# Kernel tuning notes

Hardware: AMD Instinct MI355X
Metric: run time of the kernel (lower is better)

The kernel has to match this reference:

```python
import jax, jax.numpy as jnp
import numpy as np
import math

D_MODEL = 1024
NUM_HEADS = 16
MAX_LEN = 2048
D_HEAD = D_MODEL // NUM_HEADS
BATCH = 2
SEQ = 2048


def setup_inputs() -> dict:
    root = jax.random.key(0)
    ks = jax.random.split(root, 10)
    s = 1.0 / math.sqrt(D_MODEL)
    return {
        "query": jax.random.normal(ks[0], (BATCH, SEQ, D_MODEL), jnp.float32),
        "key": jax.random.normal(ks[1], (BATCH, SEQ, D_MODEL), jnp.float32),
        "value": jax.random.normal(ks[2], (BATCH, SEQ, D_MODEL), jnp.float32),
        "Wq": jax.random.normal(ks[3], (D_MODEL, D_MODEL), jnp.float32) * s,
        "bq": jax.random.normal(ks[4], (D_MODEL,), jnp.float32) * s,
        "Wk": jax.random.normal(ks[5], (D_MODEL, D_MODEL), jnp.float32) * s,
        "bk": jax.random.normal(ks[6], (D_MODEL,), jnp.float32) * s,
        "Wv": jax.random.normal(ks[7], (D_MODEL, D_MODEL), jnp.float32) * s,
        "bv": jax.random.normal(ks[8], (D_MODEL,), jnp.float32) * s,
        "Er": jax.random.normal(ks[9], (MAX_LEN, D_HEAD), jnp.float32),
    }


def _skew(QEr):
    # QEr: [B, H, S, S] -> pad one zero column on the left, reshape, drop first row
    B, H, R, C = QEr.shape
    padded = jnp.pad(QEr, ((0, 0), (0, 0), (0, 0), (1, 0)))  # [B,H,R,C+1]
    reshaped = padded.reshape(B, H, C + 1, R)
    return reshaped[:, :, 1:, :]  # [B,H,R,C] == Srel


def reference(query, key, value, Wq, bq, Wk, bk, Wv, bv, Er):
    B, S, D = query.shape
    H, dh = NUM_HEADS, D_HEAD
    # nn.Linear: x @ W.T + b
    q = (jnp.einsum("bsd,ed->bse", query, Wq) + bq).reshape(B, S, H, dh).transpose(0, 2, 1, 3)  # [B,H,S,dh]
    k = (jnp.einsum("bsd,ed->bse", key, Wk) + bk).reshape(B, S, H, dh).transpose(0, 2, 1, 3)
    v = (jnp.einsum("bsd,ed->bse", value, Wv) + bv).reshape(B, S, H, dh).transpose(0, 2, 1, 3)
    start = MAX_LEN - S
    Er_s = Er[start:, :]  # [S, dh]
    QEr = jnp.einsum("bhsd,ld->bhsl", q, Er_s)  # [B,H,S,S]
    Srel = _skew(QEr)
    QK = jnp.einsum("bhsd,bhtd->bhst", q, k)
    attn = (QK + Srel) / math.sqrt(dh)
    causal = jnp.tril(jnp.ones((S, S), dtype=bool))
    attn = jnp.where(causal[None, None], attn, -jnp.inf)
    attn = jax.nn.softmax(attn, axis=-1)
    out = jnp.einsum("bhst,bhtd->bhsd", attn, v)  # [B,H,S,dh]
    out = out.transpose(0, 2, 1, 3).reshape(B, S, D)
    return out  # dropout is identity in eval mode
```

## Files before the change

kernel.cpp:

```cpp
#include <hip/hip_runtime.h>
#include <hip/hip_bf16.h>

typedef __attribute__((ext_vector_type(8))) short bf16x8;
typedef __attribute__((ext_vector_type(4))) float f32x4;

#define DEVI __device__ __forceinline__

constexpr int SEQ_   = 2048;
constexpr int HEADS  = 16;
constexpr int DHEAD  = 64;
constexpr int DMODEL = 1024;

DEVI unsigned short f2bf(float x) {
  __hip_bfloat16 h = __float2bfloat16(x);
  return __builtin_bit_cast(unsigned short, h);
}

DEVI f32x4 MFMA(bf16x8 a, bf16x8 b, f32x4 c) {
  return __builtin_amdgcn_mfma_f32_16x16x32_bf16(a, b, c, 0, 0, 0);
}

__global__ void conv3_kernel(const float* s0, const float* s1, const float* s2,
                             unsigned short* d0, unsigned short* d1, unsigned short* d2,
                             int n) {
  const float* s = (blockIdx.y == 0) ? s0 : (blockIdx.y == 1) ? s1 : s2;
  unsigned short* d = (blockIdx.y == 0) ? d0 : (blockIdx.y == 1) ? d1 : d2;
  int i = (blockIdx.x * 256 + threadIdx.x) * 8;
  if (i >= n) return;
  const float4* p = (const float4*)(s + i);
  float4 v0 = p[0], v1 = p[1];
  union { unsigned short u[8]; bf16x8 v; } t;
  t.u[0] = f2bf(v0.x); t.u[1] = f2bf(v0.y); t.u[2] = f2bf(v0.z); t.u[3] = f2bf(v0.w);
  t.u[4] = f2bf(v1.x); t.u[5] = f2bf(v1.y); t.u[6] = f2bf(v1.z); t.u[7] = f2bf(v1.w);
  *(bf16x8*)(d + i) = t.v;
}

__global__ void conv4_kernel(const float* s0, const float* s1, const float* s2,
                             const float* s3,
                             unsigned short* d0, unsigned short* d1,
                             unsigned short* d2, unsigned short* d3,
                             int n_w, int n_e) {
  const int y = blockIdx.y;
  const float* s = (y == 0) ? s0 : (y == 1) ? s1 : (y == 2) ? s2 : s3;
  unsigned short* d = (y == 0) ? d0 : (y == 1) ? d1 : (y == 2) ? d2 : d3;
  const int n = (y == 3) ? n_e : n_w;
  int i = (blockIdx.x * 256 + threadIdx.x) * 8;
  if (i >= n) return;
  const float4* p = (const float4*)(s + i);
  float4 v0 = p[0], v1 = p[1];
  union { unsigned short u[8]; bf16x8 v; } t;
  t.u[0] = f2bf(v0.x); t.u[1] = f2bf(v0.y); t.u[2] = f2bf(v0.z); t.u[3] = f2bf(v0.w);
  t.u[4] = f2bf(v1.x); t.u[5] = f2bf(v1.y); t.u[6] = f2bf(v1.z); t.u[7] = f2bf(v1.w);
  *(bf16x8*)(d + i) = t.v;
}

__global__ __launch_bounds__(256) void proj3_kernel(
    const unsigned short* __restrict__ X0, const unsigned short* __restrict__ X1,
    const unsigned short* __restrict__ X2,
    const unsigned short* __restrict__ W0, const unsigned short* __restrict__ W1,
    const unsigned short* __restrict__ W2,
    const float* __restrict__ bi0, const float* __restrict__ bi1,
    const float* __restrict__ bi2,
    unsigned short* __restrict__ o0, unsigned short* __restrict__ o1,
    unsigned short* __restrict__ o2) {
  const int z = blockIdx.z;
  const unsigned short* X = (z == 0) ? X0 : (z == 1) ? X1 : X2;
  const unsigned short* W = (z == 0) ? W0 : (z == 1) ? W1 : W2;
  const float* bias        = (z == 0) ? bi0 : (z == 1) ? bi1 : bi2;
  unsigned short* out      = (z == 0) ? o0 : (z == 1) ? o1 : o2;

  __shared__ unsigned short Abuf[2][128 * 32];
  __shared__ unsigned short Bbuf[2][128 * 32];
  const int tid  = threadIdx.x;
  const int lane = tid & 63, wv = tid >> 6;
  const int q = lane >> 4, r = lane & 15;
  const int wrow = wv >> 1, wcol = wv & 1;
  const int rowA0 = blockIdx.x * 128, colB0 = blockIdx.y * 128;

  const char* Ag = (const char*)(X + (size_t)rowA0 * DMODEL);
  const char* Bg = (const char*)(W + (size_t)colB0 * DMODEL);

  f32x4 acc[4][4] = {};

  auto stage = [&](int ks, int buf) {
    const int koff = ks * 64;
#pragma unroll
    for (int i = 0; i < 2; ++i) {
      const int b   = (i * 256 + tid) * 16;
      const int row = b >> 6, col = b & 63;
      __builtin_amdgcn_global_load_lds(
          (const __attribute__((address_space(1))) void*)(Ag + (size_t)row * (DMODEL * 2) + koff + col),
          (__attribute__((address_space(3))) void*)((char*)&Abuf[buf][0] + i * 4096 + wv * 1024),
          16, 0, 0);
      __builtin_amdgcn_global_load_lds(
          (const __attribute__((address_space(1))) void*)(Bg + (size_t)row * (DMODEL * 2) + koff + col),
          (__attribute__((address_space(3))) void*)((char*)&Bbuf[buf][0] + i * 4096 + wv * 1024),
          16, 0, 0);
    }
  };

  stage(0, 0);
  for (int ks = 0; ks < 32; ++ks) {
    __syncthreads();
    if (ks + 1 < 32) stage(ks + 1, (ks + 1) & 1);
    const unsigned short* A  = &Abuf[ks & 1][0];
    const unsigned short* Bt = &Bbuf[ks & 1][0];
    bf16x8 af[4], bfr[4];
#pragma unroll
    for (int t = 0; t < 4; ++t) {
      af[t]  = *(const bf16x8*)(A  + (wrow * 64 + t * 16 + r) * 32 + q * 8);
      bfr[t] = *(const bf16x8*)(Bt + (wcol * 64 + t * 16 + r) * 32 + q * 8);
    }
#pragma unroll
    for (int m = 0; m < 4; ++m)
#pragma unroll
      for (int n = 0; n < 4; ++n)
        acc[m][n] = MFMA(af[m], bfr[n], acc[m][n]);
  }

#pragma unroll
  for (int m = 0; m < 4; ++m) {
#pragma unroll
    for (int n = 0; n < 4; ++n) {
      const int e  = colB0 + wcol * 64 + n * 16 + r;
      const float bv = bias[e];
      const int h = e >> 6, dd = e & 63;
      const int nrow0 = rowA0 + wrow * 64 + m * 16 + q * 4;
      const int bb = nrow0 >> 11, ss0 = nrow0 & 2047;
      const size_t bh = (size_t)(bb * HEADS + h);
      if (z == 0) {
#pragma unroll
        for (int j = 0; j < 4; ++j)
          out[(bh * SEQ_ + (ss0 + j)) * DHEAD + dd] = f2bf((acc[m][n][j] + bv) * 0.125f);
      } else if (z == 1) {
#pragma unroll
        for (int j = 0; j < 4; ++j) {
          const int s = ss0 + j;
          const size_t off = (bh * 64 + (size_t)(s >> 5)) * 2048
                           + (size_t)(((dd >> 5) * 2 + ((s >> 4) & 1)) * 512)
                           + (size_t)(((((dd & 31) >> 3) << 4) + (s & 15)) * 8)
                           + (dd & 7);
          out[off] = f2bf(acc[m][n][j] + bv);
        }
      } else {
        union { unsigned short u[4]; uint2 v; } pk;
#pragma unroll
        for (int j = 0; j < 4; ++j) pk.u[j] = f2bf(acc[m][n][j] + bv);
        const size_t off = (bh * 64 + (size_t)(ss0 >> 5)) * 2048
                         + (size_t)((dd >> 4) * 512)
                         + (size_t)(((((ss0 & 31) >> 3) << 4) + (dd & 15)) * 8)
                         + (ss0 & 7);
        *(uint2*)&out[off] = pk.v;
      }
    }
  }
}

struct ErF { bf16x8 e10, e11, e20, e21; };

__global__ __launch_bounds__(512, 4) void attn_kernel(
    const unsigned short* __restrict__ qb, const unsigned short* __restrict__ kt,
    const unsigned short* __restrict__ vt, const unsigned short* __restrict__ Er,
    float* __restrict__ out) {
  __shared__ unsigned short k_lds[2][2048];
  __shared__ unsigned short v_lds[2][2048];
  __shared__ unsigned short p_lds[8][16][40];

  const int tid  = threadIdx.x;
  const int lane = tid & 63, wv = tid >> 6;
  const int q = lane >> 4, r = lane & 15;

  const int lid = blockIdx.x;
  const int xcd = lid & 7, idx = lid >> 3;
  const int bh  = (xcd << 2) | (idx & 3);
  const int T   = 15 - (idx >> 2);
  const int s0  = T * 128 + wv * 16;
  const int nIter = 4 * T + 4;
  const int bb = bh >> 4, hh = bh & 15;

  const unsigned short* qbh = qb + (size_t)bh * SEQ_ * DHEAD;
  const char* ktb = (const char*)(kt + (size_t)bh * 64 * 2048);
  const char* vtb = (const char*)(vt + (size_t)bh * 64 * 2048);
  const f32x4 zero4 = {0.f, 0.f, 0.f, 0.f};

  const bool isK = (tid < 256);
  const char* sbase = isK ? ktb : vtb;
  const int subt = tid & 255;

  auto stage = [&](int tile, int buf) {
    char* dst = (char*)(isK ? &k_lds[buf][0] : &v_lds[buf][0]) + (wv & 3) * 1024;
    __builtin_amdgcn_global_load_lds(
        (const __attribute__((address_space(1))) void*)(sbase + (size_t)tile * 4096 + subt * 16),
        (__attribute__((address_space(3))) void*)dst, 16, 0, 0);
  };

  auto loadE = [&](ErF& e, int it2) {
    const int lb = 2032 + it2 * 32 - s0;
    int l1 = lb + 16 + r; l1 = l1 < 2047 ? l1 : 2047;
    int l2 = lb + 32 + r; l2 = l2 < 2047 ? l2 : 2047;
    e.e10 = *(const bf16x8*)(Er + (size_t)l1 * DHEAD + q * 8);
    e.e11 = *(const bf16x8*)(Er + (size_t)l1 * DHEAD + 32 + q * 8);
    e.e20 = *(const bf16x8*)(Er + (size_t)l2 * DHEAD + q * 8);
    e.e21 = *(const bf16x8*)(Er + (size_t)l2 * DHEAD + 32 + q * 8);
  };

  stage(0, 0);
  bf16x8 qf0 = *(const bf16x8*)(qbh + (size_t)(s0 + r) * DHEAD + q * 8);
  bf16x8 qf1 = *(const bf16x8*)(qbh + (size_t)(s0 + r) * DHEAD + 32 + q * 8);

  f32x4 oacc[4] = {};
  float lpart[4] = {0.f, 0.f, 0.f, 0.f};
  f32x4 qer0;
  {
    const int l0 = 2032 - s0 + r;
    bf16x8 e00 = *(const bf16x8*)(Er + (size_t)l0 * DHEAD + q * 8);
    bf16x8 e01 = *(const bf16x8*)(Er + (size_t)l0 * DHEAD + 32 + q * 8);
    qer0 = MFMA(qf1, e01, MFMA(qf0, e00, zero4));
  }

  auto body = [&](int it, int cur, const ErF& e) {
    const int t0 = it * 32;
    if (t0 > s0 + 15) return;
    const unsigned short* KL = &k_lds[cur][0];
    const unsigned short* VL = &v_lds[cur][0];
    bf16x8 kf00 = *(const bf16x8*)(KL + lane * 8);
    bf16x8 kf10 = *(const bf16x8*)(KL + 512 + lane * 8);
    bf16x8 kf01 = *(const bf16x8*)(KL + 1024 + lane * 8);
    bf16x8 kf11 = *(const bf16x8*)(KL + 1536 + lane * 8);

    __builtin_amdgcn_s_setprio(1);
    f32x4 s40  = MFMA(qf1, kf01, MFMA(qf0, kf00, zero4));
    f32x4 s41  = MFMA(qf1, kf11, MFMA(qf0, kf10, zero4));
    f32x4 qer1 = MFMA(qf1, e.e11, MFMA(qf0, e.e10, zero4));
    f32x4 qer2 = MFMA(qf1, e.e21, MFMA(qf0, e.e20, zero4));
    __builtin_amdgcn_s_setprio(0);

    const int d0 = t0 - s0;
#pragma unroll
    for (int j = 0; j < 4; ++j) {
      const int sl = q * 4 + j;
      const int idxw = r + 15 - sl;
      const int srcl = (q << 4) | (idxw & 15);
      const float g0s = __shfl(qer0[j], srcl);
      const float g1s = __shfl(qer1[j], srcl);
      const float g2s = __shfl(qer2[j], srcl);
      const bool lo = (idxw < 16);
      const float sv0 = s40[j] + (lo ? g0s : g1s);
      const float sv1 = s41[j] + (lo ? g1s : g2s);
      const int a = sl - r;
      const float p0 = (a >= d0)      ? __expf(sv0) : 0.f;
      const float p1 = (a >= d0 + 16) ? __expf(sv1) : 0.f;
      lpart[j] += p0 + p1;
      p_lds[wv][sl][r]      = f2bf(p0);
      p_lds[wv][sl][16 + r] = f2bf(p1);
    }

    bf16x8 pf  = *(const bf16x8*)(&p_lds[wv][r][0] + q * 8);
    bf16x8 vf0 = *(const bf16x8*)(VL + lane * 8);
    bf16x8 vf1 = *(const bf16x8*)(VL + 512 + lane * 8);
    bf16x8 vf2 = *(const bf16x8*)(VL + 1024 + lane * 8);
    bf16x8 vf3 = *(const bf16x8*)(VL + 1536 + lane * 8);
    __builtin_amdgcn_s_setprio(1);
    oacc[0] = MFMA(pf, vf0, oacc[0]);
    oacc[1] = MFMA(pf, vf1, oacc[1]);
    oacc[2] = MFMA(pf, vf2, oacc[2]);
    oacc[3] = MFMA(pf, vf3, oacc[3]);
    __builtin_amdgcn_s_setprio(0);
    qer0 = qer2;
  };

  ErF eA, eB;
  loadE(eA, 0);
  int it = 0;
  while (true) {
    __syncthreads();
    if (it + 1 < nIter) { stage(it + 1, 1); loadE(eB, it + 1); }
    body(it, 0, eA);
    if (++it >= nIter) break;
    __syncthreads();
    if (it + 1 < nIter) { stage(it + 1, 0); loadE(eA, it + 1); }
    body(it, 1, eB);
    if (++it >= nIter) break;
  }

#pragma unroll
  for (int j = 0; j < 4; ++j) {
    float ls = lpart[j];
#pragma unroll
    for (int d = 1; d < 16; d <<= 1) ls += __shfl_xor(ls, d);
    const float inv = 1.0f / ls;
    const int ss = s0 + q * 4 + j;
#pragma unroll
    for (int dc = 0; dc < 4; ++dc) {
      const int dd = dc * 16 + r;
      out[((size_t)(bb * SEQ_ + ss)) * DMODEL + hh * DHEAD + dd] = oacc[dc][j] * inv;
    }
  }
}

extern "C" void kernel_launch(void* const* d_in, const int* in_sizes, int n_in,
                              void* d_out, int out_size, void* d_ws, size_t ws_size,
                              hipStream_t stream) {
  const float* query = (const float*)d_in[0];
  const float* key   = (const float*)d_in[1];
  const float* value = (const float*)d_in[2];
  const float* Wq    = (const float*)d_in[3];
  const float* bq    = (const float*)d_in[4];
  const float* Wk    = (const float*)d_in[5];
  const float* bk    = (const float*)d_in[6];
  const float* Wv    = (const float*)d_in[7];
  const float* bv    = (const float*)d_in[8];
  const float* Er    = (const float*)d_in[9];

  char* ws = (char*)d_ws;
  unsigned short* qb   = (unsigned short*)(ws + (0u  << 20));
  unsigned short* ktil = (unsigned short*)(ws + (8u  << 20));
  unsigned short* vtil = (unsigned short*)(ws + (16u << 20));
  unsigned short* Xq   = (unsigned short*)(ws + (32u << 20));
  unsigned short* Xk   = (unsigned short*)(ws + (40u << 20));
  unsigned short* Xv   = (unsigned short*)(ws + (48u << 20));
  unsigned short* Wqb  = (unsigned short*)(ws + (56u << 20));
  unsigned short* Wkb  = (unsigned short*)(ws + (58u << 20));
  unsigned short* Wvb  = (unsigned short*)(ws + (60u << 20));
  unsigned short* Erb  = (unsigned short*)(ws + (62u << 20));

  conv3_kernel<<<dim3(2048, 3), 256, 0, stream>>>(query, key, value, Xq, Xk, Xv,
                                                  2 * SEQ_ * DMODEL);
  conv4_kernel<<<dim3(512, 4), 256, 0, stream>>>(Wq, Wk, Wv, Er,
                                                 Wqb, Wkb, Wvb, Erb,
                                                 DMODEL * DMODEL, SEQ_ * DHEAD);

  proj3_kernel<<<dim3(32, 8, 3), 256, 0, stream>>>(Xq, Xk, Xv, Wqb, Wkb, Wvb,
                                                   bq, bk, bv, qb, ktil, vtil);

  attn_kernel<<<dim3(512), 512, 0, stream>>>(qb, ktil, vtil, Erb, (float*)d_out);
}
```

Before: 163.8 us.

## Retile attention to 32-row waves, 64-key tiles, and triple-buffered KV loads

The attention kernel now uses 4 waves of 32 query rows each, in place of 8 waves of 16 rows, and processes 64 keys per iteration instead of 32. Each K/V fragment loaded from LDS is therefore reused across two row tiles, and there are half as many iterations and barriers. KV staging moves to a 3-deep LDS ring, with a manual vmcnt wait plus s_barrier replacing __syncthreads so prefetches can stay in flight. In exchange it uses more registers and LDS, and has fewer waves per block and per CU, which may hurt latency hiding.

Result: faster. 144.5 us (-11.8%).

```diff
diff --git a/kernel.cpp b/kernel.cpp
--- a/kernel.cpp
+++ b/kernel.cpp
@@ -5,6 +5,8 @@
 typedef __attribute__((ext_vector_type(4))) float f32x4;
 
 #define DEVI __device__ __forceinline__
+#define AS1 __attribute__((address_space(1)))
+#define AS3 __attribute__((address_space(3)))
 
 constexpr int SEQ_   = 2048;
 constexpr int HEADS  = 16;
@@ -89,12 +91,12 @@
       const int b   = (i * 256 + tid) * 16;
       const int row = b >> 6, col = b & 63;
       __builtin_amdgcn_global_load_lds(
-          (const __attribute__((address_space(1))) void*)(Ag + (size_t)row * (DMODEL * 2) + koff + col),
-          (__attribute__((address_space(3))) void*)((char*)&Abuf[buf][0] + i * 4096 + wv * 1024),
+          (const AS1 void*)(Ag + (size_t)row * (DMODEL * 2) + koff + col),
+          (AS3 void*)((char*)&Abuf[buf][0] + i * 4096 + wv * 1024),
           16, 0, 0);
       __builtin_amdgcn_global_load_lds(
-          (const __attribute__((address_space(1))) void*)(Bg + (size_t)row * (DMODEL * 2) + koff + col),
-          (__attribute__((address_space(3))) void*)((char*)&Bbuf[buf][0] + i * 4096 + wv * 1024),
+          (const AS1 void*)(Bg + (size_t)row * (DMODEL * 2) + koff + col),
+          (AS3 void*)((char*)&Bbuf[buf][0] + i * 4096 + wv * 1024),
           16, 0, 0);
     }
   };
@@ -156,15 +158,13 @@
   }
 }
 
-struct ErF { bf16x8 e10, e11, e20, e21; };
-
-__global__ __launch_bounds__(512, 4) void attn_kernel(
+__global__ __launch_bounds__(256, 2) void attn_kernel(
     const unsigned short* __restrict__ qb, const unsigned short* __restrict__ kt,
     const unsigned short* __restrict__ vt, const unsigned short* __restrict__ Er,
     float* __restrict__ out) {
-  __shared__ unsigned short k_lds[2][2048];
-  __shared__ unsigned short v_lds[2][2048];
-  __shared__ unsigned short p_lds[8][16][40];
+  __shared__ unsigned short k_lds[3][4096];
+  __shared__ unsigned short v_lds[3][4096];
+  __shared__ unsigned short p_lds[4][32][72];
 
   const int tid  = threadIdx.x;
   const int lane = tid & 63, wv = tid >> 6;
@@ -174,8 +174,8 @@
   const int xcd = lid & 7, idx = lid >> 3;
   const int bh  = (xcd << 2) | (idx & 3);
   const int T   = 15 - (idx >> 2);
-  const int s0  = T * 128 + wv * 16;
-  const int nIter = 4 * T + 4;
+  const int s0  = T * 128 + wv * 32;
+  const int nIter = 2 * T + 2;
   const int bb = bh >> 4, hh = bh & 15;
 
   const unsigned short* qbh = qb + (size_t)bh * SEQ_ * DHEAD;
@@ -183,119 +183,173 @@
   const char* vtb = (const char*)(vt + (size_t)bh * 64 * 2048);
   const f32x4 zero4 = {0.f, 0.f, 0.f, 0.f};
 
-  const bool isK = (tid < 256);
-  const char* sbase = isK ? ktb : vtb;
-  const int subt = tid & 255;
-
-  auto stage = [&](int tile, int buf) {
-    char* dst = (char*)(isK ? &k_lds[buf][0] : &v_lds[buf][0]) + (wv & 3) * 1024;
-    __builtin_amdgcn_global_load_lds(
-        (const __attribute__((address_space(1))) void*)(sbase + (size_t)tile * 4096 + subt * 16),
-        (__attribute__((address_space(3))) void*)dst, 16, 0, 0);
+  const char* sgbase = (wv < 2) ? ktb : vtb;
+  char* sdst0 = (char*)((wv < 2) ? &k_lds[0][0] : &v_lds[0][0]);
+  const int shalf = (wv & 1) * 4096;
+  const int soff  = lane * 16;
+
+  auto stageKV = [&](int it, int buf) {
+    const int g = (it < nIter) ? it : nIter - 1;
+    const char* src = sgbase + (size_t)g * 8192 + shalf + soff;
+    char* dst = sdst0 + buf * 8192 + shalf;
+#pragma unroll
+    for (int c = 0; c < 4; ++c)
+      __builtin_amdgcn_global_load_lds((const AS1 void*)(src + c * 1024),
+                                       (AS3 void*)(dst + c * 1024), 16, 0, 0);
   };
 
-  auto loadE = [&](ErF& e, int it2) {
-    const int lb = 2032 + it2 * 32 - s0;
-    int l1 = lb + 16 + r; l1 = l1 < 2047 ? l1 : 2047;
-    int l2 = lb + 32 + r; l2 = l2 < 2047 ? l2 : 2047;
-    e.e10 = *(const bf16x8*)(Er + (size_t)l1 * DHEAD + q * 8);
-    e.e11 = *(const bf16x8*)(Er + (size_t)l1 * DHEAD + 32 + q * 8);
-    e.e20 = *(const bf16x8*)(Er + (size_t)l2 * DHEAD + q * 8);
-    e.e21 = *(const bf16x8*)(Er + (size_t)l2 * DHEAD + 32 + q * 8);
+  struct ErSet { bf16x8 e[8]; };
+  auto loadE = [&](ErSet& es, int it) {
+    const int lb = 2016 + it * 64 - s0;
+#pragma unroll
+    for (int mi = 0; mi < 4; ++mi) {
+      int l = lb + 32 + mi * 16 + r;
+      l = l < 2047 ? l : 2047;
+      es.e[mi * 2 + 0] = *(const bf16x8*)(Er + (size_t)l * DHEAD + q * 8);
+      es.e[mi * 2 + 1] = *(const bf16x8*)(Er + (size_t)l * DHEAD + 32 + q * 8);
+    }
   };
 
-  stage(0, 0);
-  bf16x8 qf0 = *(const bf16x8*)(qbh + (size_t)(s0 + r) * DHEAD + q * 8);
-  bf16x8 qf1 = *(const bf16x8*)(qbh + (size_t)(s0 + r) * DHEAD + 32 + q * 8);
-
-  f32x4 oacc[4] = {};
-  float lpart[4] = {0.f, 0.f, 0.f, 0.f};
-  f32x4 qer0;
+  bf16x8 qf[2][2];
+#pragma unroll
+  for (int rt = 0; rt < 2; ++rt) {
+    qf[rt][0] = *(const bf16x8*)(qbh + (size_t)(s0 + rt * 16 + r) * DHEAD + q * 8);
+    qf[rt][1] = *(const bf16x8*)(qbh + (size_t)(s0 + rt * 16 + r) * DHEAD + 32 + q * 8);
+  }
+  stageKV(0, 0);
+
+  f32x4 qer[2][6];
   {
-    const int l0 = 2032 - s0 + r;
-    bf16x8 e00 = *(const bf16x8*)(Er + (size_t)l0 * DHEAD + q * 8);
-    bf16x8 e01 = *(const bf16x8*)(Er + (size_t)l0 * DHEAD + 32 + q * 8);
-    qer0 = MFMA(qf1, e01, MFMA(qf0, e00, zero4));
-  }
-
-  auto body = [&](int it, int cur, const ErF& e) {
-    const int t0 = it * 32;
-    if (t0 > s0 + 15) return;
+    const int lb = 2016 - s0;
+#pragma unroll
+    for (int m = 0; m < 2; ++m) {
+      const int l = lb + m * 16 + r;
+      bf16x8 e0 = *(const bf16x8*)(Er + (size_t)l * DHEAD + q * 8);
+      bf16x8 e1 = *(const bf16x8*)(Er + (size_t)l * DHEAD + 32 + q * 8);
+#pragma unroll
+      for (int rt = 0; rt < 2; ++rt)
+        qer[rt][m] = MFMA(qf[rt][1], e1, MFMA(qf[rt][0], e0, zero4));
+    }
+  }
+
+  f32x4 oacc[2][4] = {};
+  float lpart[2][4] = {};
+
+  ErSet eA, eB;
+  loadE(eA, 0);
+
+  auto body = [&](int it, int cur, const ErSet& es) {
+    const int t0 = it * 64;
+    if (t0 > s0 + 31) return;
     const unsigned short* KL = &k_lds[cur][0];
     const unsigned short* VL = &v_lds[cur][0];
-    bf16x8 kf00 = *(const bf16x8*)(KL + lane * 8);
-    bf16x8 kf10 = *(const bf16x8*)(KL + 512 + lane * 8);
-    bf16x8 kf01 = *(const bf16x8*)(KL + 1024 + lane * 8);
-    bf16x8 kf11 = *(const bf16x8*)(KL + 1536 + lane * 8);
-
+
+    bf16x8 kf[4][2];
+#pragma unroll
+    for (int ct = 0; ct < 4; ++ct)
+#pragma unroll
+      for (int kc = 0; kc < 2; ++kc)
+        kf[ct][kc] = *(const bf16x8*)(KL + (ct >> 1) * 2048 + (kc * 2 + (ct & 1)) * 512 + lane * 8);
+
+    f32x4 s4[2][4];
     __builtin_amdgcn_s_setprio(1);
-    f32x4 s40  = MFMA(qf1, kf01, MFMA(qf0, kf00, zero4));
-    f32x4 s41  = MFMA(qf1, kf11, MFMA(qf0, kf10, zero4));
-    f32x4 qer1 = MFMA(qf1, e.e11, MFMA(qf0, e.e10, zero4));
-    f32x4 qer2 = MFMA(qf1, e.e21, MFMA(qf0, e.e20, zero4));
+#pragma unroll
+    for (int rt = 0; rt < 2; ++rt)
+#pragma unroll
+      for (int ct = 0; ct < 4; ++ct)
+        s4[rt][ct] = MFMA(qf[rt][1], kf[ct][1], MFMA(qf[rt][0], kf[ct][0], zero4));
+#pragma unroll
+    for (int rt = 0; rt < 2; ++rt)
+#pragma unroll
+      for (int mi = 0; mi < 4; ++mi)
+        qer[rt][2 + mi] = MFMA(qf[rt][1], es.e[mi * 2 + 1],
+                               MFMA(qf[rt][0], es.e[mi * 2 + 0], zero4));
     __builtin_amdgcn_s_setprio(0);
 
     const int d0 = t0 - s0;
 #pragma unroll
+    for (int rt = 0; rt < 2; ++rt) {
+#pragma unroll
+      for (int j = 0; j < 4; ++j) {
+        const int srcl = (q << 4) | ((15 + r - q * 4 - j) & 15);
+        float g0 = __shfl(qer[rt][1 - rt][j], srcl);
+        float g1 = __shfl(qer[rt][2 - rt][j], srcl);
+        float g2 = __shfl(qer[rt][3 - rt][j], srcl);
+        float g3 = __shfl(qer[rt][4 - rt][j], srcl);
+        float g4 = __shfl(qer[rt][5 - rt][j], srcl);
+        const bool hi = (r > q * 4 + j);
+        const float b0 = hi ? g1 : g0;
+        const float b1 = hi ? g2 : g1;
+        const float b2 = hi ? g3 : g2;
+        const float b3 = hi ? g4 : g3;
+        const int A_ = rt * 16 + q * 4 + j - r - d0;
+        const float p0 = (A_ >= 0)  ? __expf(s4[rt][0][j] + b0) : 0.f;
+        const float p1 = (A_ >= 16) ? __expf(s4[rt][1][j] + b1) : 0.f;
+        const float p2 = (A_ >= 32) ? __expf(s4[rt][2][j] + b2) : 0.f;
+        const float p3 = (A_ >= 48) ? __expf(s4[rt][3][j] + b3) : 0.f;
+        lpart[rt][j] += (p0 + p1) + (p2 + p3);
+        const int sl = rt * 16 + q * 4 + j;
+        p_lds[wv][sl][r]      = f2bf(p0);
+        p_lds[wv][sl][16 + r] = f2bf(p1);
+        p_lds[wv][sl][32 + r] = f2bf(p2);
+        p_lds[wv][sl][48 + r] = f2bf(p3);
+      }
+    }
+
+    bf16x8 vf[4][2];
+#pragma unroll
+    for (int dc = 0; dc < 4; ++dc)
+#pragma unroll
+      for (int tc = 0; tc < 2; ++tc)
+        vf[dc][tc] = *(const bf16x8*)(VL + tc * 2048 + dc * 512 + lane * 8);
+    __builtin_amdgcn_s_setprio(1);
+#pragma unroll
+    for (int rt = 0; rt < 2; ++rt) {
+      bf16x8 pf0 = *(const bf16x8*)(&p_lds[wv][rt * 16 + r][0] + q * 8);
+      bf16x8 pf1 = *(const bf16x8*)(&p_lds[wv][rt * 16 + r][0] + 32 + q * 8);
+#pragma unroll
+      for (int dc = 0; dc < 4; ++dc)
+        oacc[rt][dc] = MFMA(pf1, vf[dc][1], MFMA(pf0, vf[dc][0], oacc[rt][dc]));
+    }
+    __builtin_amdgcn_s_setprio(0);
+
+#pragma unroll
+    for (int rt = 0; rt < 2; ++rt) { qer[rt][0] = qer[rt][4]; qer[rt][1] = qer[rt][5]; }
+  };
+
+  int it = 0, cur = 0;
+  while (true) {
+    int nxt = cur + 1; if (nxt == 3) nxt = 0;
+    stageKV(it + 1, nxt);
+    loadE(eB, it + 1);
+    asm volatile("s_waitcnt vmcnt(12)\n\ts_barrier" ::: "memory");
+    body(it, cur, eA);
+    cur = nxt;
+    if (++it >= nIter) break;
+    nxt = cur + 1; if (nxt == 3) nxt = 0;
+    stageKV(it + 1, nxt);
+    loadE(eA, it + 1);
+    asm volatile("s_waitcnt vmcnt(12)\n\ts_barrier" ::: "memory");
+    body(it, cur, eB);
+    cur = nxt;
+    if (++it >= nIter) break;
+  }
+
+#pragma unroll
+  for (int rt = 0; rt < 2; ++rt)
+#pragma unroll
     for (int j = 0; j < 4; ++j) {
-      const int sl = q * 4 + j;
-      const int idxw = r + 15 - sl;
-      const int srcl = (q << 4) | (idxw & 15);
-      const float g0s = __shfl(qer0[j], srcl);
-      const float g1s = __shfl(qer1[j], srcl);
-      const float g2s = __shfl(qer2[j], srcl);
-      const bool lo = (idxw < 16);
-      const float sv0 = s40[j] + (lo ? g0s : g1s);
-      const float sv1 = s41[j] + (lo ? g1s : g2s);
-      const int a = sl - r;
-      const float p0 = (a >= d0)      ? __expf(sv0) : 0.f;
-      const float p1 = (a >= d0 + 16) ? __expf(sv1) : 0.f;
-      lpart[j] += p0 + p1;
-      p_lds[wv][sl][r]      = f2bf(p0);
-      p_lds[wv][sl][16 + r] = f2bf(p1);
-    }
-
-    bf16x8 pf  = *(const bf16x8*)(&p_lds[wv][r][0] + q * 8);
-    bf16x8 vf0 = *(const bf16x8*)(VL + lane * 8);
-    bf16x8 vf1 = *(const bf16x8*)(VL + 512 + lane * 8);
-    bf16x8 vf2 = *(const bf16x8*)(VL + 1024 + lane * 8);
-    bf16x8 vf3 = *(const bf16x8*)(VL + 1536 + lane * 8);
-    __builtin_amdgcn_s_setprio(1);
-    oacc[0] = MFMA(pf, vf0, oacc[0]);
-    oacc[1] = MFMA(pf, vf1, oacc[1]);
-    oacc[2] = MFMA(pf, vf2, oacc[2]);
-    oacc[3] = MFMA(pf, vf3, oacc[3]);
-    __builtin_amdgcn_s_setprio(0);
-    qer0 = qer2;
-  };
-
-  ErF eA, eB;
-  loadE(eA, 0);
-  int it = 0;
-  while (true) {
-    __syncthreads();
-    if (it + 1 < nIter) { stage(it + 1, 1); loadE(eB, it + 1); }
-    body(it, 0, eA);
-    if (++it >= nIter) break;
-    __syncthreads();
-    if (it + 1 < nIter) { stage(it + 1, 0); loadE(eA, it + 1); }
-    body(it, 1, eB);
-    if (++it >= nIter) break;
-  }
-
-#pragma unroll
-  for (int j = 0; j < 4; ++j) {
-    float ls = lpart[j];
-#pragma unroll
-    for (int d = 1; d < 16; d <<= 1) ls += __shfl_xor(ls, d);
-    const float inv = 1.0f / ls;
-    const int ss = s0 + q * 4 + j;
-#pragma unroll
-    for (int dc = 0; dc < 4; ++dc) {
-      const int dd = dc * 16 + r;
-      out[((size_t)(bb * SEQ_ + ss)) * DMODEL + hh * DHEAD + dd] = oacc[dc][j] * inv;
-    }
-  }
+      float ls = lpart[rt][j];
+#pragma unroll
+      for (int d = 1; d < 16; d <<= 1) ls += __shfl_xor(ls, d);
+      const float inv = 1.0f / ls;
+      const int ss = s0 + rt * 16 + q * 4 + j;
+#pragma unroll
+      for (int dc = 0; dc < 4; ++dc) {
+        const int dd = dc * 16 + r;
+        out[((size_t)(bb * SEQ_ + ss)) * DMODEL + hh * DHEAD + dd] = oacc[rt][dc][j] * inv;
+      }
+    }
 }
 
 extern "C" void kernel_launch(void* const* d_in, const int* in_sizes, int n_in,
@@ -333,5 +387,5 @@
   proj3_kernel<<<dim3(32, 8, 3), 256, 0, stream>>>(Xq, Xk, Xv, Wqb, Wkb, Wvb,
                                                    bq, bk, bv, qb, ktil, vtil);
 
-  attn_kernel<<<dim3(512), 512, 0, stream>>>(qb, ktil, vtil, Erb, (float*)d_out);
-}
+  attn_kernel<<<dim3(512), 256, 0, stream>>>(qb, ktil, vtil, Erb, (float*)d_out);
+}
```
